# Kernel optimization log

Hardware: AMD Instinct MI355X
Metric: run time of the kernel (lower is better)

The kernel has to match this reference:

```python
import jax, jax.numpy as jnp
import numpy as np

B, S, DM, H, HD = 2, 2048, 1024, 16, 64
MEM_SIZE = 1000
K_SIMILAR, K_CONTIG = 8, 2
K_TOTAL = K_SIMILAR + K_CONTIG  # 10 memory tokens
NEG = -1e9


def setup_inputs() -> dict:
    key = jax.random.key(0)
    k1, k2, k3, k4, k5, k6 = jax.random.split(key, 6)
    inputs = jax.random.normal(k1, (B, S, DM), dtype=jnp.float32)
    attention_mask = jnp.ones((B, S), dtype=jnp.float32)
    Wq = jax.random.normal(k2, (DM, H * HD), dtype=jnp.float32) * 0.02
    Wk = jax.random.normal(k3, (DM, H * HD), dtype=jnp.float32) * 0.02
    Wv = jax.random.normal(k4, (DM, H * HD), dtype=jnp.float32) * 0.02
    Wo = jax.random.normal(k5, (H * HD, DM), dtype=jnp.float32) * 0.02
    events = jax.random.normal(k6, (MEM_SIZE, H * HD), dtype=jnp.float32) * 0.02
    return {"inputs": inputs, "attention_mask": attention_mask,
            "Wq": Wq, "Wk": Wk, "Wv": Wv, "Wo": Wo, "events": events}


def _forward(inputs, attention_mask, Wq, Wk, Wv, Wo, events):
    # projections (no bias), split heads: [B, H, S, HD]
    q = (inputs @ Wq).reshape(B, S, H, HD).transpose(0, 2, 1, 3)
    k = (inputs @ Wk).reshape(B, S, H, HD).transpose(0, 2, 1, 3)
    v = (inputs @ Wv).reshape(B, S, H, HD).transpose(0, 2, 1, 3)

    # --- episodic retrieval: cosine top-k of last-token key vs events ---
    qvec = k[:, :, -1, :].reshape(B, H * HD)                       # [B, D]
    qn = qvec / (jnp.linalg.norm(qvec, axis=-1, keepdims=True) + 1e-8)
    en = events / (jnp.linalg.norm(events, axis=-1, keepdims=True) + 1e-8)
    sims = qn @ en.T                                               # [B, M]
    _, topk_idx = jax.lax.top_k(sims, K_TOTAL)                     # [B, K]
    retrieved = events[topk_idx]                                   # [B, K, D]
    retrieved_k = retrieved.reshape(B, K_TOTAL, H, HD).transpose(0, 2, 1, 3)  # [B,H,K,HD]
    retrieved_v = retrieved_k                                      # non-differential path

    aug_k = jnp.concatenate([retrieved_k, k], axis=2)              # [B,H,K+S,HD]
    aug_v = jnp.concatenate([retrieved_v, v], axis=2)

    # --- ALiBi bias: slopes * (pos_i - pos_j) on original cols, 0 on memory cols ---
    slopes = 2.0 ** (-8.0 * jnp.arange(1, H + 1, dtype=jnp.float32) / H)  # [H]
    positions = jnp.arange(S, dtype=jnp.float32)
    pos_diff = positions[:, None] - positions[None, :]             # [S, S]
    alibi = slopes[:, None, None] * pos_diff                       # [H, S, S]
    alibi = jnp.concatenate([jnp.zeros((H, S, K_TOTAL), jnp.float32), alibi], axis=-1)

    # --- causal mask: -1e9 strictly-upper on original cols, 0 on memory cols ---
    tri = jnp.where(jnp.arange(S)[None, :] > jnp.arange(S)[:, None], NEG, 0.0)  # [S,S]
    causal = jnp.concatenate([jnp.zeros((S, K_TOTAL), jnp.float32), tri], axis=-1)

    # --- padding mask: memory tokens always attendable ---
    aug_mask = jnp.concatenate([jnp.ones((B, K_TOTAL), jnp.float32), attention_mask], axis=-1)
    mask_bias = (1.0 - aug_mask)[:, None, None, :] * NEG           # [B,1,1,K+S]

    scores = jnp.einsum("bhqd,bhkd->bhqk", q, aug_k) / np.sqrt(HD)
    scores = scores + alibi[None] + causal[None, None] + mask_bias
    attn = jax.nn.softmax(scores, axis=-1)
    out = jnp.einsum("bhqk,bhkd->bhqd", attn, aug_v)               # [B,H,S,HD]
    out = out.transpose(0, 2, 1, 3).reshape(B, S, H * HD)
    return out @ Wo


def reference(inputs, attention_mask, Wq, Wk, Wv, Wo, events):
    return _forward(inputs, attention_mask, Wq, Wk, Wv, Wo, events)
```

## Files before the change

### kernel.cpp

```cpp
#include <hip/hip_runtime.h>
#include <hip/hip_bf16.h>
#include <math.h>

#define B_   2
#define S_   2048
#define DM_  1024
#define H_   16
#define HD_  64
#define MEM_ 1000
#define KTOT 10
#define NROW (B_ * S_)
#define NEG9 (-1e9f)
#define LDK  72
#define NITEMS 1024

typedef __attribute__((ext_vector_type(8))) short short8;
typedef __attribute__((ext_vector_type(4))) float f32x4;

__device__ __forceinline__ void gll16(const __hip_bfloat16* g, __hip_bfloat16* l) {
    __builtin_amdgcn_global_load_lds(
        (const __attribute__((address_space(1))) void*)g,
        (__attribute__((address_space(3))) void*)l, 16, 0, 0);
}

__global__ __launch_bounds__(256) void prep(const float* __restrict__ inputs,
                                            const float* __restrict__ Wq,
                                            const float* __restrict__ Wk,
                                            const float* __restrict__ Wv,
                                            const float* __restrict__ Wo,
                                            __hip_bfloat16* __restrict__ Ax,
                                            __hip_bfloat16* __restrict__ Wt,
                                            float* __restrict__ lk,
                                            int* __restrict__ ctr) {
    const int bx = blockIdx.x, tid = threadIdx.x;
    if (bx == 0 && tid == 0) *ctr = 0;

    if (bx < 2048) {
        const size_t i = ((size_t)bx * 256 + tid) * 8;
        float4 a = *(const float4*)&inputs[i];
        float4 b = *(const float4*)&inputs[i + 4];
        alignas(16) __hip_bfloat16 t[8];
        t[0] = __float2bfloat16(a.x); t[1] = __float2bfloat16(a.y);
        t[2] = __float2bfloat16(a.z); t[3] = __float2bfloat16(a.w);
        t[4] = __float2bfloat16(b.x); t[5] = __float2bfloat16(b.y);
        t[6] = __float2bfloat16(b.z); t[7] = __float2bfloat16(b.w);
        *(short8*)&Ax[i] = *(short8*)t;
        return;
    }
    if (bx < 3072) {
        const int idx = bx - 2048;
        const int g = idx >> 8, rem = idx & 255;
        const float* W = (g == 0) ? Wq : (g == 1) ? Wk : (g == 2) ? Wv : Wo;
        const int n0 = (rem & 15) * 64, k0 = (rem >> 4) * 64;
        __shared__ float T[64][65];
        {
            const int r = tid >> 4, c4 = (tid & 15) * 4;
#pragma unroll
            for (int p = 0; p < 4; ++p) {
                float4 v = *(const float4*)&W[(size_t)(k0 + r + p * 16) * 1024 + n0 + c4];
                T[r + p * 16][c4 + 0] = v.x; T[r + p * 16][c4 + 1] = v.y;
                T[r + p * 16][c4 + 2] = v.z; T[r + p * 16][c4 + 3] = v.w;
            }
        }
        __syncthreads();
        {
            const int n = tid >> 3, off = (tid & 7) * 8;
#pragma unroll
            for (int p = 0; p < 2; ++p) {
                const int nn = n + p * 32;
                alignas(16) __hip_bfloat16 t[8];
#pragma unroll
                for (int j = 0; j < 8; ++j) t[j] = __float2bfloat16(T[off + j][nn]);
                *(short8*)&Wt[((size_t)(g * 1024 + n0 + nn)) * 1024 + k0 + off] = *(short8*)t;
            }
        }
        return;
    }
    {
        const int idx = bx - 3072;
        const int xblk = idx & 15, b = idx >> 4;
        const int cl = tid & 63;
        const int col = xblk * 64 + cl;
        const int kq = tid >> 6;
        __shared__ float xr[1024];
        __shared__ float part[4][64];
        for (int i = tid; i < 1024; i += 256)
            xr[i] = inputs[((size_t)(b * S_ + S_ - 1)) * 1024 + i];
        __syncthreads();
        float acc = 0.f;
#pragma unroll 4
        for (int k = kq * 256; k < kq * 256 + 256; ++k)
            acc += xr[k] * Wk[(size_t)k * 1024 + col];
        part[kq][cl] = acc;
        __syncthreads();
        if (tid < 64)
            lk[b * 1024 + xblk * 64 + tid] =
                part[0][tid] + part[1][tid] + part[2][tid] + part[3][tid];
    }
}

__device__ __forceinline__ void store_out(__hip_bfloat16* p, float x) { *p = __float2bfloat16(x); }
__device__ __forceinline__ void store_out(float* p, float x) { *p = x; }

template <typename OutT>
__global__ __launch_bounds__(256) void gemm_mfma(const __hip_bfloat16* __restrict__ A,
                                                 const __hip_bfloat16* __restrict__ Bt,
                                                 OutT* __restrict__ C, int ldc) {
    __shared__ __hip_bfloat16 As[128 * 32];
    __shared__ __hip_bfloat16 Bs[128 * 32];
    const int tid = threadIdx.x;
    const int wave = tid >> 6, lane = tid & 63;
    const int quad = lane >> 4, lm = lane & 15;
    const int wr = wave >> 1, wc = wave & 1;
    const int m0 = blockIdx.y * 128, n0 = blockIdx.x * 128;

    const int r0 = tid >> 2, c0 = (tid & 3) * 8;
    const __hip_bfloat16* ga0 = &A[(size_t)(m0 + r0) * 1024 + c0];
    const __hip_bfloat16* ga1 = &A[(size_t)(m0 + 64 + r0) * 1024 + c0];
    const __hip_bfloat16* gb0 = &Bt[(size_t)(n0 + r0) * 1024 + c0];
    const __hip_bfloat16* gb1 = &Bt[(size_t)(n0 + 64 + r0) * 1024 + c0];
    __hip_bfloat16* la0 = &As[(wave * 64) * 8];
    __hip_bfloat16* la1 = &As[(256 + wave * 64) * 8];
    __hip_bfloat16* lb0 = &Bs[(wave * 64) * 8];
    __hip_bfloat16* lb1 = &Bs[(256 + wave * 64) * 8];

    f32x4 acc[4][4];
#pragma unroll
    for (int i = 0; i < 4; ++i)
#pragma unroll
        for (int j = 0; j < 4; ++j) acc[i][j] = (f32x4){0.f, 0.f, 0.f, 0.f};

    for (int k0 = 0; k0 < 1024; k0 += 32) {
        __syncthreads();
        gll16(ga0 + k0, la0);
        gll16(ga1 + k0, la1);
        gll16(gb0 + k0, lb0);
        gll16(gb1 + k0, lb1);
        __syncthreads();
        short8 af[4], bf4[4];
#pragma unroll
        for (int mt = 0; mt < 4; ++mt)
            af[mt] = *(const short8*)&As[(wr * 64 + mt * 16 + lm) * 32 + quad * 8];
#pragma unroll
        for (int nt = 0; nt < 4; ++nt)
            bf4[nt] = *(const short8*)&Bs[(wc * 64 + nt * 16 + lm) * 32 + quad * 8];
#pragma unroll
        for (int mt = 0; mt < 4; ++mt)
#pragma unroll
            for (int nt = 0; nt < 4; ++nt)
                acc[mt][nt] = __builtin_amdgcn_mfma_f32_16x16x32_bf16(
                    af[mt], bf4[nt], acc[mt][nt], 0, 0, 0);
    }
#pragma unroll
    for (int mt = 0; mt < 4; ++mt)
#pragma unroll
        for (int nt = 0; nt < 4; ++nt) {
            const int col = n0 + wc * 64 + nt * 16 + lm;
#pragma unroll
            for (int i = 0; i < 4; ++i) {
                const int row = m0 + wr * 64 + mt * 16 + quad * 4 + i;
                store_out(&C[(size_t)row * ldc + col], acc[mt][nt][i]);
            }
        }
}

__global__ __launch_bounds__(256) void sims_kernel(const float* __restrict__ lk,
                                                   const float* __restrict__ events,
                                                   float* __restrict__ sims) {
    const int b = blockIdx.y;
    const int tid = threadIdx.x;
    const int wave = tid >> 6, lane = tid & 63;
    __shared__ float qv[1024];
    for (int i = tid; i < 1024; i += 256)
        qv[i] = lk[b * 1024 + i];
    __syncthreads();

    const int m = blockIdx.x * 4 + wave;
    if (m >= MEM_) return;
    const float* ev = &events[(size_t)m * 1024];
    float dot = 0.f, nrm = 0.f;
    for (int d = lane; d < 1024; d += 64) {
        float e = ev[d];
        dot += qv[d] * e;
        nrm += e * e;
    }
    for (int off = 32; off; off >>= 1) {
        dot += __shfl_down(dot, off);
        nrm += __shfl_down(nrm, off);
    }
    if (lane == 0) sims[b * 1024 + m] = dot / (sqrtf(nrm) + 1e-8f);
}

__global__ __launch_bounds__(256) void topk10_kernel(const float* __restrict__ sims,
                                                     int* __restrict__ topk) {
    const int b = blockIdx.x;
    const int tid = threadIdx.x;
    __shared__ float sv[1024];
    __shared__ float bv[256];
    __shared__ int   bi[256];
    for (int m = tid; m < 1024; m += 256)
        sv[m] = (m < MEM_) ? sims[b * 1024 + m] : -INFINITY;
    __syncthreads();

    for (int it = 0; it < KTOT; ++it) {
        float best = -INFINITY; int besti = 0x7fffffff;
        for (int m = tid; m < 1024; m += 256) {
            float s = sv[m];
            if (s > best || (s == best && m < besti)) { best = s; besti = m; }
        }
        bv[tid] = best; bi[tid] = besti;
        __syncthreads();
        for (int stride = 128; stride; stride >>= 1) {
            if (tid < stride) {
                float ov = bv[tid + stride]; int oi = bi[tid + stride];
                if (ov > bv[tid] || (ov == bv[tid] && oi < bi[tid])) {
                    bv[tid] = ov; bi[tid] = oi;
                }
            }
            __syncthreads();
        }
        if (tid == 0) { topk[b * KTOT + it] = bi[0]; sv[bi[0]] = -INFINITY; }
        __syncthreads();
    }
}

__global__ __launch_bounds__(256) void attn_mfma(
        const __hip_bfloat16* __restrict__ qkv,
        const float* __restrict__ events,
        const int* __restrict__ topk,
        const float* __restrict__ amask,
        __hip_bfloat16* __restrict__ out,
        int* __restrict__ ctr) {
    const int tid = threadIdx.x;
    const int wave = tid >> 6, lane = tid & 63;
    const int quad = lane >> 4, lm = lane & 15;

    const __hip_bfloat16* qf = qkv;
    const __hip_bfloat16* kf = qkv + 1024;
    const __hip_bfloat16* vf = qkv + 2048;

    __shared__ __hip_bfloat16 Qs[64 * LDK];
    __shared__ __hip_bfloat16 Ks[64 * LDK];
    __shared__ __hip_bfloat16 Vt[64 * LDK];
    __shared__ __hip_bfloat16 Ps[64 * LDK];
    __shared__ float colb[64];
    __shared__ float redb[4];
    __shared__ int sItem;

    const int va = tid & 31, vdc = tid >> 5;
    const int vtok0 = va * 2, vd0 = vdc * 8;

    for (;;) {
        __syncthreads();
        if (tid == 0) sItem = atomicAdd(ctr, 1);
        __syncthreads();
        const int n = sItem;
        if (n >= NITEMS) break;

        const int qt = 31 - (n >> 5);
        const int q0 = qt * 64;
        const int inner = n & 31;
        const int h = 15 - ((inner >> 1) & 15);
        const int b = inner & 1;
        const float slope = exp2f(-0.5f * (float)(h + 1));

        {
            const __hip_bfloat16* src = &qf[((size_t)(b * S_ + q0)) * 3072 + h * 64];
#pragma unroll
            for (int u = 0; u < 2; ++u) {
                int c = tid * 2 + u, row = c >> 3, off = (c & 7) * 8;
                *(short8*)&Qs[row * LDK + off] =
                    *(const short8*)&src[(size_t)row * 3072 + off];
            }
        }
        for (int i = tid * 8; i < 64 * LDK; i += 256 * 8)
            *(int4*)&Vt[i] = make_int4(0, 0, 0, 0);
        __syncthreads();
        if (tid < 80) {
            const int tok = tid >> 3, d0 = (tid & 7) * 8;
            const int ev = topk[b * KTOT + tok];
            const float* es = &events[(size_t)ev * 1024 + h * 64 + d0];
#pragma unroll
            for (int j = 0; j < 8; ++j) {
                __hip_bfloat16 x = __float2bfloat16(es[j]);
                Ks[tok * LDK + d0 + j] = x;
                Vt[(d0 + j) * LDK + tok] = x;
            }
        }
        __syncthreads();

        float m_[4], l_[4], mshift[4];
        f32x4 Oa[4];
#pragma unroll
        for (int i = 0; i < 4; ++i) {
            m_[i] = -INFINITY; l_[i] = 0.f;
            mshift[i] = -slope * (float)(q0 + wave * 16 + quad * 4 + i);
        }
#pragma unroll
        for (int nt = 0; nt < 4; ++nt) Oa[nt] = (f32x4){0.f, 0.f, 0.f, 0.f};

        short8 pk[2], pv0, pv1;
        float pam = 1.f;
        auto prefetchKV = [&](int kt) {
            const __hip_bfloat16* ks = &kf[((size_t)(b * S_ + kt * 64)) * 3072 + h * 64];
#pragma unroll
            for (int u = 0; u < 2; ++u) {
                int c = tid * 2 + u, row = c >> 3, off = (c & 7) * 8;
                pk[u] = *(const short8*)&ks[(size_t)row * 3072 + off];
            }
            const __hip_bfloat16* v0 =
                &vf[((size_t)(b * S_ + kt * 64 + vtok0)) * 3072 + h * 64 + vd0];
            pv0 = *(const short8*)v0;
            pv1 = *(const short8*)(v0 + 3072);
            if (tid < 64) pam = amask[b * S_ + kt * 64 + tid];
        };
        auto stageKV = [&](int kt) {
#pragma unroll
            for (int u = 0; u < 2; ++u) {
                int c = tid * 2 + u, row = c >> 3, off = (c & 7) * 8;
                *(short8*)&Ks[row * LDK + off] = pk[u];
            }
#pragma unroll
            for (int j = 0; j < 8; ++j) {
                short2 pr; pr.x = pv0[j]; pr.y = pv1[j];
                *(short2*)&Vt[(vd0 + j) * LDK + vtok0] = pr;
            }
            if (tid < 64)
                colb[tid] = fmaf(-slope, (float)(kt * 64 + tid), (1.f - pam) * NEG9);
        };

        auto qk = [&](f32x4* sa) {
#pragma unroll
            for (int nt = 0; nt < 4; ++nt) sa[nt] = (f32x4){0.f, 0.f, 0.f, 0.f};
#pragma unroll
            for (int ks2 = 0; ks2 < 2; ++ks2) {
                short8 aq = *(const short8*)&Qs[(wave * 16 + lm) * LDK + ks2 * 32 + quad * 8];
#pragma unroll
                for (int nt = 0; nt < 4; ++nt) {
                    short8 bk = *(const short8*)&Ks[(nt * 16 + lm) * LDK + ks2 * 32 + quad * 8];
                    sa[nt] = __builtin_amdgcn_mfma_f32_16x16x32_bf16(aq, bk, sa[nt], 0, 0, 0);
                }
            }
        };
        auto pv = [&]() {
#pragma unroll
            for (int ks2 = 0; ks2 < 2; ++ks2) {
                short8 ap = *(const short8*)&Ps[(wave * 16 + lm) * LDK + ks2 * 32 + quad * 8];
#pragma unroll
                for (int nt = 0; nt < 4; ++nt) {
                    short8 bv = *(const short8*)&Vt[(nt * 16 + lm) * LDK + ks2 * 32 + quad * 8];
                    Oa[nt] = __builtin_amdgcn_mfma_f32_16x16x32_bf16(ap, bv, Oa[nt], 0, 0, 0);
                }
            }
        };

        auto softmax_online = [&](const f32x4* sa, int kt, bool diag) {
            float cb[4];
            if (kt >= 0) {
#pragma unroll
                for (int nt = 0; nt < 4; ++nt) cb[nt] = colb[nt * 16 + lm];
            }
#pragma unroll
            for (int i = 0; i < 4; ++i) {
                const int lr = wave * 16 + quad * 4 + i;
                const int rg = q0 + lr;
                float s[4];
#pragma unroll
                for (int nt = 0; nt < 4; ++nt) {
                    const int cc = nt * 16 + lm;
                    if (kt < 0) {
                        s[nt] = (cc < KTOT) ? fmaf(sa[nt][i], 0.125f, mshift[i]) : NEG9;
                    } else {
                        float v = fmaf(sa[nt][i], 0.125f, cb[nt]);
                        s[nt] = (diag && kt * 64 + cc > rg) ? NEG9 : v;
                    }
                }
                float rmax = fmaxf(fmaxf(s[0], s[1]), fmaxf(s[2], s[3]));
#pragma unroll
                for (int off = 1; off < 16; off <<= 1)
                    rmax = fmaxf(rmax, __shfl_xor(rmax, off, 16));
                const float newm = fmaxf(m_[i], rmax);
                const float al = __expf(m_[i] - newm);
                float p[4], ps = 0.f;
#pragma unroll
                for (int nt = 0; nt < 4; ++nt) {
                    p[nt] = __expf(s[nt] - newm);
                    ps += p[nt];
                }
#pragma unroll
                for (int off = 1; off < 16; off <<= 1)
                    ps += __shfl_xor(ps, off, 16);
                l_[i] = l_[i] * al + ps;
                m_[i] = newm;
#pragma unroll
                for (int nt = 0; nt < 4; ++nt) {
                    Oa[nt][i] *= al;
                    Ps[lr * LDK + nt * 16 + lm] = __float2bfloat16(p[nt]);
                }
            }
        };

        auto softmax_fast = [&](const f32x4* sa, int cbase, bool diag) {
            float cb[4];
#pragma unroll
            for (int nt = 0; nt < 4; ++nt) cb[nt] = colb[nt * 16 + lm];
#pragma unroll
            for (int i = 0; i < 4; ++i) {
                const int lr = wave * 16 + quad * 4 + i;
                const float cm = m_[i];
                float p[4];
#pragma unroll
                for (int nt = 0; nt < 4; ++nt)
                    p[nt] = __expf(fmaf(sa[nt][i], 0.125f, cb[nt]) - cm);
                if (diag) {
                    const int rg = q0 + lr;
#pragma unroll
                    for (int nt = 0; nt < 4; ++nt)
                        if (cbase + nt * 16 + lm > rg) p[nt] = 0.f;
                }
                float ps = (p[0] + p[1]) + (p[2] + p[3]);
#pragma unroll
                for (int off = 1; off < 16; off <<= 1)
                    ps += __shfl_xor(ps, off, 16);
                l_[i] += ps;
#pragma unroll
                for (int nt = 0; nt < 4; ++nt)
                    Ps[lr * LDK + nt * 16 + lm] = __float2bfloat16(p[nt]);
            }
        };

        prefetchKV(0);
        {
            f32x4 sa[4];
            qk(sa);
            softmax_online(sa, -1, false);
            pv();
        }
        __syncthreads();
        stageKV(0);
        if (qt >= 1) prefetchKV(1);
        __syncthreads();
        {
            f32x4 sa[4];
            qk(sa);
            softmax_online(sa, 0, qt == 0);
            pv();
        }

        int ktend = 0;
        if (qt >= 1) {
            float mloc = fminf(fminf(m_[0], m_[1]), fminf(m_[2], m_[3]));
#pragma unroll
            for (int off = 1; off < 64; off <<= 1)
                mloc = fminf(mloc, __shfl_xor(mloc, off, 64));
            if (lane == 0) redb[wave] = mloc;
            __syncthreads();
            const float mmin = fminf(fminf(redb[0], redb[1]), fminf(redb[2], redb[3]));
            ktend = min(qt, (int)((118.f - mmin) / (64.f * slope)));
        }
        for (int kt = 1; kt <= ktend; ++kt) {
            __syncthreads();
            stageKV(kt);
            if (kt < ktend) prefetchKV(kt + 1);
            __syncthreads();
            f32x4 sa[4];
            qk(sa);
            softmax_fast(sa, kt * 64, kt == qt);
            pv();
        }

#pragma unroll
        for (int i = 0; i < 4; ++i) {
            const int lr = wave * 16 + quad * 4 + i;
            const float inv = 1.f / l_[i];
            __hip_bfloat16* dst = &out[((size_t)(b * S_ + q0 + lr)) * 1024 + h * 64 + lm];
#pragma unroll
            for (int nt = 0; nt < 4; ++nt)
                dst[nt * 16] = __float2bfloat16(Oa[nt][i] * inv);
        }
    }
}

extern "C" void kernel_launch(void* const* d_in, const int* in_sizes, int n_in,
                              void* d_out, int out_size, void* d_ws, size_t ws_size,
                              hipStream_t stream) {
    const float* inputs = (const float*)d_in[0];
    const float* amask  = (const float*)d_in[1];
    const float* Wq     = (const float*)d_in[2];
    const float* Wk     = (const float*)d_in[3];
    const float* Wv     = (const float*)d_in[4];
    const float* Wo     = (const float*)d_in[5];
    const float* events = (const float*)d_in[6];
    float* out = (float*)d_out;

    __hip_bfloat16* Ax  = (__hip_bfloat16*)d_ws;
    __hip_bfloat16* Wt  = Ax + (size_t)NROW * 1024;
    __hip_bfloat16* qkv = Wt + (size_t)4096 * 1024;
    __hip_bfloat16* ao  = qkv + (size_t)NROW * 3072;
    float* lk   = (float*)(ao + (size_t)NROW * 1024);
    float* sims = lk + 2 * 1024;
    int* topk   = (int*)(sims + 2 * 1024);
    int* ctr    = topk + B_ * KTOT;

    dim3 blk(256);
    prep<<<3104, blk, 0, stream>>>(inputs, Wq, Wk, Wv, Wo, Ax, Wt, lk, ctr);
    sims_kernel<<<dim3(250, B_), blk, 0, stream>>>(lk, events, sims);
    topk10_kernel<<<B_, 256, 0, stream>>>(sims, topk);
    gemm_mfma<__hip_bfloat16><<<dim3(24, 32), blk, 0, stream>>>(Ax, Wt, qkv, 3072);
    attn_mfma<<<768, blk, 0, stream>>>(qkv, events, topk, amask, ao, ctr);
    gemm_mfma<float><<<dim3(8, 32), blk, 0, stream>>>(
        ao, Wt + (size_t)3072 * 1024, out, 1024);
}
```

Baseline: 256.4 us.

## Compute softmax row sums via extra MFMA ones column; keep Q in registers; wave-level top-k

The attention kernel drops the per-row shuffle reductions for the softmax denominator. It appends a 16-row block to the transposed V tile whose first row is all ones, so a fifth MFMA accumulates the row sums of the rounded P values; the sum is read back with a shuffle at the end. Q fragments are now loaded straight into registers instead of being staged in LDS, which saves LDS traffic and space. The top-10 kernel is rewritten as a single-wave register-and-shuffle reduction with no shared memory or barriers. The costs are one extra MFMA per k-step, more accumulator registers, and a denominator computed from bf16-rounded probabilities.

Result: faster. 244.2 us (-4.8%).

```diff
diff --git a/kernel.cpp b/kernel.cpp
--- a/kernel.cpp
+++ b/kernel.cpp
@@ -191,36 +191,31 @@
     if (lane == 0) sims[b * 1024 + m] = dot / (sqrtf(nrm) + 1e-8f);
 }
 
-__global__ __launch_bounds__(256) void topk10_kernel(const float* __restrict__ sims,
-                                                     int* __restrict__ topk) {
+__global__ __launch_bounds__(64) void topk10_kernel(const float* __restrict__ sims,
+                                                    int* __restrict__ topk) {
     const int b = blockIdx.x;
-    const int tid = threadIdx.x;
-    __shared__ float sv[1024];
-    __shared__ float bv[256];
-    __shared__ int   bi[256];
-    for (int m = tid; m < 1024; m += 256)
-        sv[m] = (m < MEM_) ? sims[b * 1024 + m] : -INFINITY;
-    __syncthreads();
-
+    const int lane = threadIdx.x;
+    const int base = lane * 16;
+    float v[16];
+#pragma unroll
+    for (int j = 0; j < 16; ++j) {
+        const int m = base + j;
+        v[j] = (m < MEM_) ? sims[b * 1024 + m] : -INFINITY;
+    }
     for (int it = 0; it < KTOT; ++it) {
-        float best = -INFINITY; int besti = 0x7fffffff;
-        for (int m = tid; m < 1024; m += 256) {
-            float s = sv[m];
-            if (s > best || (s == best && m < besti)) { best = s; besti = m; }
-        }
-        bv[tid] = best; bi[tid] = besti;
-        __syncthreads();
-        for (int stride = 128; stride; stride >>= 1) {
-            if (tid < stride) {
-                float ov = bv[tid + stride]; int oi = bi[tid + stride];
-                if (ov > bv[tid] || (ov == bv[tid] && oi < bi[tid])) {
-                    bv[tid] = ov; bi[tid] = oi;
-                }
-            }
-            __syncthreads();
-        }
-        if (tid == 0) { topk[b * KTOT + it] = bi[0]; sv[bi[0]] = -INFINITY; }
-        __syncthreads();
+        float best = -INFINITY; int bi = 0x7fffffff;
+#pragma unroll
+        for (int j = 0; j < 16; ++j)
+            if (v[j] > best) { best = v[j]; bi = base + j; }
+        for (int off = 32; off; off >>= 1) {
+            const float ob = __shfl_xor(best, off);
+            const int   oi = __shfl_xor(bi, off);
+            if (ob > best || (ob == best && oi < bi)) { best = ob; bi = oi; }
+        }
+        if (lane == 0) topk[b * KTOT + it] = bi;
+#pragma unroll
+        for (int j = 0; j < 16; ++j)
+            if (base + j == bi) v[j] = -INFINITY;
     }
 }
 
@@ -239,9 +234,8 @@
     const __hip_bfloat16* kf = qkv + 1024;
     const __hip_bfloat16* vf = qkv + 2048;
 
-    __shared__ __hip_bfloat16 Qs[64 * LDK];
     __shared__ __hip_bfloat16 Ks[64 * LDK];
-    __shared__ __hip_bfloat16 Vt[64 * LDK];
+    __shared__ __hip_bfloat16 Vt[80 * LDK];
     __shared__ __hip_bfloat16 Ps[64 * LDK];
     __shared__ float colb[64];
     __shared__ float redb[4];
@@ -249,6 +243,11 @@
 
     const int va = tid & 31, vdc = tid >> 5;
     const int vtok0 = va * 2, vd0 = vdc * 8;
+
+    for (int i = tid; i < 16 * LDK; i += 256) {
+        const int r = i / LDK;
+        Vt[64 * LDK + i] = __float2bfloat16(r == 0 ? 1.0f : 0.0f);
+    }
 
     for (;;) {
         __syncthreads();
@@ -264,14 +263,12 @@
         const int b = inner & 1;
         const float slope = exp2f(-0.5f * (float)(h + 1));
 
+        short8 qa[2];
         {
-            const __hip_bfloat16* src = &qf[((size_t)(b * S_ + q0)) * 3072 + h * 64];
-#pragma unroll
-            for (int u = 0; u < 2; ++u) {
-                int c = tid * 2 + u, row = c >> 3, off = (c & 7) * 8;
-                *(short8*)&Qs[row * LDK + off] =
-                    *(const short8*)&src[(size_t)row * 3072 + off];
-            }
+            const __hip_bfloat16* qsrc =
+                &qf[((size_t)(b * S_ + q0 + wave * 16 + lm)) * 3072 + h * 64 + quad * 8];
+            qa[0] = *(const short8*)qsrc;
+            qa[1] = *(const short8*)(qsrc + 32);
         }
         for (int i = tid * 8; i < 64 * LDK; i += 256 * 8)
             *(int4*)&Vt[i] = make_int4(0, 0, 0, 0);
@@ -289,15 +286,15 @@
         }
         __syncthreads();
 
-        float m_[4], l_[4], mshift[4];
-        f32x4 Oa[4];
+        float m_[4], mshift[4];
+        f32x4 Oa[5];
 #pragma unroll
         for (int i = 0; i < 4; ++i) {
-            m_[i] = -INFINITY; l_[i] = 0.f;
+            m_[i] = -INFINITY;
             mshift[i] = -slope * (float)(q0 + wave * 16 + quad * 4 + i);
         }
 #pragma unroll
-        for (int nt = 0; nt < 4; ++nt) Oa[nt] = (f32x4){0.f, 0.f, 0.f, 0.f};
+        for (int nt = 0; nt < 5; ++nt) Oa[nt] = (f32x4){0.f, 0.f, 0.f, 0.f};
 
         short8 pk[2], pv0, pv1;
         float pam = 1.f;
@@ -334,11 +331,10 @@
             for (int nt = 0; nt < 4; ++nt) sa[nt] = (f32x4){0.f, 0.f, 0.f, 0.f};
 #pragma unroll
             for (int ks2 = 0; ks2 < 2; ++ks2) {
-                short8 aq = *(const short8*)&Qs[(wave * 16 + lm) * LDK + ks2 * 32 + quad * 8];
 #pragma unroll
                 for (int nt = 0; nt < 4; ++nt) {
                     short8 bk = *(const short8*)&Ks[(nt * 16 + lm) * LDK + ks2 * 32 + quad * 8];
-                    sa[nt] = __builtin_amdgcn_mfma_f32_16x16x32_bf16(aq, bk, sa[nt], 0, 0, 0);
+                    sa[nt] = __builtin_amdgcn_mfma_f32_16x16x32_bf16(qa[ks2], bk, sa[nt], 0, 0, 0);
                 }
             }
         };
@@ -347,7 +343,7 @@
             for (int ks2 = 0; ks2 < 2; ++ks2) {
                 short8 ap = *(const short8*)&Ps[(wave * 16 + lm) * LDK + ks2 * 32 + quad * 8];
 #pragma unroll
-                for (int nt = 0; nt < 4; ++nt) {
+                for (int nt = 0; nt < 5; ++nt) {
                     short8 bv = *(const short8*)&Vt[(nt * 16 + lm) * LDK + ks2 * 32 + quad * 8];
                     Oa[nt] = __builtin_amdgcn_mfma_f32_16x16x32_bf16(ap, bv, Oa[nt], 0, 0, 0);
                 }
@@ -381,22 +377,13 @@
                     rmax = fmaxf(rmax, __shfl_xor(rmax, off, 16));
                 const float newm = fmaxf(m_[i], rmax);
                 const float al = __expf(m_[i] - newm);
-                float p[4], ps = 0.f;
-#pragma unroll
-                for (int nt = 0; nt < 4; ++nt) {
-                    p[nt] = __expf(s[nt] - newm);
-                    ps += p[nt];
-                }
-#pragma unroll
-                for (int off = 1; off < 16; off <<= 1)
-                    ps += __shfl_xor(ps, off, 16);
-                l_[i] = l_[i] * al + ps;
                 m_[i] = newm;
 #pragma unroll
-                for (int nt = 0; nt < 4; ++nt) {
+                for (int nt = 0; nt < 4; ++nt)
+                    Ps[lr * LDK + nt * 16 + lm] = __float2bfloat16(__expf(s[nt] - newm));
+#pragma unroll
+                for (int nt = 0; nt < 5; ++nt)
                     Oa[nt][i] *= al;
-                    Ps[lr * LDK + nt * 16 + lm] = __float2bfloat16(p[nt]);
-                }
             }
         };
 
@@ -418,11 +405,6 @@
                     for (int nt = 0; nt < 4; ++nt)
                         if (cbase + nt * 16 + lm > rg) p[nt] = 0.f;
                 }
-                float ps = (p[0] + p[1]) + (p[2] + p[3]);
-#pragma unroll
-                for (int off = 1; off < 16; off <<= 1)
-                    ps += __shfl_xor(ps, off, 16);
-                l_[i] += ps;
 #pragma unroll
                 for (int nt = 0; nt < 4; ++nt)
                     Ps[lr * LDK + nt * 16 + lm] = __float2bfloat16(p[nt]);
@@ -472,7 +454,8 @@
 #pragma unroll
         for (int i = 0; i < 4; ++i) {
             const int lr = wave * 16 + quad * 4 + i;
-            const float inv = 1.f / l_[i];
+            const float l = __shfl(Oa[4][i], (lane & 48));
+            const float inv = 1.f / l;
             __hip_bfloat16* dst = &out[((size_t)(b * S_ + q0 + lr)) * 1024 + h * 64 + lm];
 #pragma unroll
             for (int nt = 0; nt < 4; ++nt)
@@ -505,7 +488,7 @@
     dim3 blk(256);
     prep<<<3104, blk, 0, stream>>>(inputs, Wq, Wk, Wv, Wo, Ax, Wt, lk, ctr);
     sims_kernel<<<dim3(250, B_), blk, 0, stream>>>(lk, events, sims);
-    topk10_kernel<<<B_, 256, 0, stream>>>(sims, topk);
+    topk10_kernel<<<B_, 64, 0, stream>>>(sims, topk);
     gemm_mfma<__hip_bfloat16><<<dim3(24, 32), blk, 0, stream>>>(Ax, Wt, qkv, 3072);
     attn_mfma<<<768, blk, 0, stream>>>(qkv, events, topk, amask, ao, ctr);
     gemm_mfma<float><<<dim3(8, 32), blk, 0, stream>>>(
```
